# Kernel optimization log

Hardware: AMD Instinct MI355X
Metric: run time of the kernel (lower is better)

## Reference

```python
import jax, jax.numpy as jnp
import numpy as np

B, T, U = 4, 256, 64
D_ENC, D_DEC = 640, 640
INNER, VOCAB = 640, 1024


def setup_inputs() -> dict:
    key = jax.random.key(0)
    k1, k2, k3, k4, k5, k6 = jax.random.split(key, 6)
    return {
        "enc_state": jax.random.normal(k1, (B, T, D_ENC), jnp.float32),
        "dec_state": jax.random.normal(k2, (B, U, D_DEC), jnp.float32),
        # forward_layer: Linear(input_size=1280 -> inner=640); stored as [in, out]
        "w1": jax.random.normal(k3, (D_ENC + D_DEC, INNER), jnp.float32) * (1.0 / np.sqrt(D_ENC + D_DEC)),
        "b1": jax.random.normal(k4, (INNER,), jnp.float32) * 0.02,
        # project_layer: Linear(inner=640 -> vocab=1024)
        "w2": jax.random.normal(k5, (INNER, VOCAB), jnp.float32) * (1.0 / np.sqrt(INNER)),
        "b2": jax.random.normal(k6, (VOCAB,), jnp.float32) * 0.02,
    }


def reference(enc_state, dec_state, w1, b1, w2, b2):
    # Linear on concat([enc, dec]) == enc @ w1[:D_enc] + dec @ w1[D_enc:]
    # (same math as the torch repeat+cat+Linear, without materializing the
    #  [B,T,U,2D] concatenated grid)
    d_enc = enc_state.shape[-1]
    enc_proj = jnp.einsum('btd,dh->bth', enc_state, w1[:d_enc])   # [B,T,H]
    dec_proj = jnp.einsum('bud,dh->buh', dec_state, w1[d_enc:])   # [B,U,H]
    h = jnp.tanh(enc_proj[:, :, None, :] + dec_proj[:, None, :, :] + b1)  # [B,T,U,H]
    return jnp.einsum('btuh,hv->btuv', h, w2) + b2                # [B,T,U,V]
```

## Files before the change

kernel.cpp:

```cpp
#include <hip/hip_runtime.h>
#include <hip/hip_bf16.h>


typedef __attribute__((ext_vector_type(4))) float  f32x4;
typedef __attribute__((ext_vector_type(8))) __bf16 bf16x8;
typedef __attribute__((ext_vector_type(8))) unsigned short us8;

#define INNER 640
#define VOCAB 1024
#define M_TOT 65536
#define RE 1024
#define RD 256

#define ENCP_B (RE * INNER * 4)
#define DECP_B (RD * INNER * 4)
#define W2BT_B (VOCAB * INNER * 2)
#define HB_B   ((size_t)M_TOT * INNER * 2)
#define OFF_DECP ((size_t)ENCP_B)
#define OFF_W2BT (OFF_DECP + DECP_B)
#define OFF_HB   (OFF_W2BT + W2BT_B)
#define NEED_FULL (OFF_HB + HB_B)

__device__ __forceinline__ unsigned short f2bf(float f) {
    unsigned int u = __float_as_uint(f);
    u = (u + 0x7FFFu + ((u >> 16) & 1u)) >> 16;
    return (unsigned short)u;
}

__device__ __forceinline__ float fast_tanh(float x) {
    float e = __builtin_amdgcn_exp2f(x * 2.8853900817779268f);
    return 1.0f - 2.0f * __builtin_amdgcn_rcpf(e + 1.0f);
}

__device__ __forceinline__ void gl_lds16(const void* g, void* l) {
    __builtin_amdgcn_global_load_lds(
        (__attribute__((address_space(1))) void*)g,
        (__attribute__((address_space(3))) void*)l, 16, 0, 0);
}

__global__ __launch_bounds__(256) void prep_kernel(
        const float* __restrict__ enc, const float* __restrict__ dec,
        const float* __restrict__ w1, const float* __restrict__ b1,
        const float* __restrict__ w2,
        float* __restrict__ encp, float* __restrict__ decp,
        unsigned short* __restrict__ w2bT) {
    __shared__ __align__(16) char smem[64 * 65 * 4];
    int bx = blockIdx.x;
    int t = threadIdx.x;
    if (bx < 200) {
        float (*At)[68] = (float(*)[68])smem;
        float (*Bt)[68] = (float(*)[68])(smem + 16 * 68 * 4);
        const float* Ap; float* Op; const float* Wp; int mt, nt; bool isdec;
        if (bx < 160) { isdec = false; mt = bx / 10; nt = bx % 10; Ap = enc; Op = encp; Wp = w1; }
        else { isdec = true; int i = bx - 160; mt = i / 10; nt = i % 10; Ap = dec; Op = decp; Wp = w1 + 640 * 640; }
        int m0 = mt * 64, n0 = nt * 64;
        int tx = t & 15, ty = t >> 4;
        int ar = t >> 2, ac = t & 3;
        int br = t >> 4, bc = t & 15;
        float acc[4][4] = {};
        for (int k0 = 0; k0 < 640; k0 += 16) {
            f32x4 av = *(const f32x4*)&Ap[(m0 + ar) * 640 + k0 + ac * 4];
            f32x4 bv = *(const f32x4*)&Wp[(k0 + br) * 640 + n0 + bc * 4];
            __syncthreads();
            At[ac * 4 + 0][ar] = av[0]; At[ac * 4 + 1][ar] = av[1];
            At[ac * 4 + 2][ar] = av[2]; At[ac * 4 + 3][ar] = av[3];
            *(f32x4*)&Bt[br][bc * 4] = bv;
            __syncthreads();
            #pragma unroll
            for (int kk = 0; kk < 16; ++kk) {
                f32x4 a = *(const f32x4*)&At[kk][ty * 4];
                f32x4 b = *(const f32x4*)&Bt[kk][tx * 4];
                #pragma unroll
                for (int i = 0; i < 4; ++i)
                    #pragma unroll
                    for (int j = 0; j < 4; ++j)
                        acc[i][j] += a[i] * b[j];
            }
        }
        f32x4 bias = {0.f, 0.f, 0.f, 0.f};
        if (isdec) bias = *(const f32x4*)&b1[n0 + tx * 4];
        #pragma unroll
        for (int i = 0; i < 4; ++i) {
            f32x4 o;
            #pragma unroll
            for (int j = 0; j < 4; ++j) o[j] = acc[i][j] + bias[j];
            *(f32x4*)&Op[(m0 + ty * 4 + i) * 640 + n0 + nt * 0 + tx * 4] = o;
        }
    } else {
        float (*tile)[65] = (float(*)[65])smem;
        int i = bx - 200;
        int kt = i % 10, ntc = i / 10;
        int k0 = kt * 64, n0 = ntc * 64;
        #pragma unroll
        for (int p = 0; p < 4; ++p) {
            int id = t + p * 256;
            int r = id >> 4, c4 = id & 15;
            f32x4 v = *(const f32x4*)&w2[(k0 + r) * 1024 + n0 + c4 * 4];
            tile[r][c4 * 4 + 0] = v[0]; tile[r][c4 * 4 + 1] = v[1];
            tile[r][c4 * 4 + 2] = v[2]; tile[r][c4 * 4 + 3] = v[3];
        }
        __syncthreads();
        #pragma unroll
        for (int p = 0; p < 2; ++p) {
            int id = t + p * 256;
            int n = id >> 3, ch = id & 7;
            us8 hv;
            #pragma unroll
            for (int q = 0; q < 8; ++q) hv[q] = f2bf(tile[ch * 8 + q][n]);
            *(us8*)&w2bT[(n0 + n) * 640 + k0 + ch * 8] = hv;
        }
    }
}

__global__ __launch_bounds__(256) void hmat_kernel(
        const float* __restrict__ encp, const float* __restrict__ decp,
        unsigned short* __restrict__ Hb) {
    int c = blockIdx.x * 256 + threadIdx.x;
    int m = c / 80;
    int kc = (c - m * 80) * 8;
    int r1 = m >> 6;
    int r2 = ((m >> 14) << 6) | (m & 63);
    const float* ep = encp + r1 * 640 + kc;
    const float* dp = decp + r2 * 640 + kc;
    f32x4 e0 = *(const f32x4*)ep, e1 = *(const f32x4*)(ep + 4);
    f32x4 d0 = *(const f32x4*)dp, d1 = *(const f32x4*)(dp + 4);
    us8 hv;
    #pragma unroll
    for (int q = 0; q < 4; ++q) hv[q] = f2bf(fast_tanh(e0[q] + d0[q]));
    #pragma unroll
    for (int q = 0; q < 4; ++q) hv[4 + q] = f2bf(fast_tanh(e1[q] + d1[q]));
    *(us8*)&Hb[(size_t)m * 640 + kc] = hv;
}

template<int FUSED>
__global__ __launch_bounds__(256) void jgemm_kernel(
        const unsigned short* __restrict__ Hb, const unsigned short* __restrict__ w2bT,
        const float* __restrict__ encp, const float* __restrict__ decp,
        const float* __restrict__ b2, float* __restrict__ out) {
    __shared__ __align__(16) unsigned short As[128 * 32];
    __shared__ __align__(16) unsigned short Bs[128 * 32];
    int bx = blockIdx.x;
    int lb = ((bx & 7) << 9) | (bx >> 3);
    int nt = lb & 7, mt = lb >> 3;
    int m0 = mt << 7, n0 = nt << 7;
    int tid = threadIdx.x;
    int lane = tid & 63, wave = tid >> 6;
    int wr = (wave >> 1) * 64, wc = (wave & 1) * 64;
    f32x4 acc[4][4] = {};
    int fr = lane & 15, fk = (lane >> 4) << 3;

    for (int kt = 0; kt < 20; ++kt) {
        int k0 = kt << 5;
        __syncthreads();
        if constexpr (!FUSED) {
            #pragma unroll
            for (int j = 0; j < 2; ++j) {
                int srow = wave * 32 + j * 16 + (lane >> 2);
                const char* ag = (const char*)Hb + (size_t)(m0 + srow) * 1280 + k0 * 2 + (lane & 3) * 16;
                const char* bg = (const char*)w2bT + (size_t)(n0 + srow) * 1280 + k0 * 2 + (lane & 3) * 16;
                gl_lds16(ag, (void*)&As[(wave * 32 + j * 16) * 32]);
                gl_lds16(bg, (void*)&Bs[(wave * 32 + j * 16) * 32]);
            }
        } else {
            int row = tid >> 1, kh = tid & 1;
            int m = m0 + row;
            int r1g = m >> 6;
            int r2g = ((m >> 14) << 6) | (m & 63);
            const float* ep = encp + r1g * 640 + k0 + kh * 16;
            const float* dp = decp + r2g * 640 + k0 + kh * 16;
            f32x4 e0 = *(const f32x4*)ep,       e1 = *(const f32x4*)(ep + 4);
            f32x4 e2 = *(const f32x4*)(ep + 8), e3 = *(const f32x4*)(ep + 12);
            f32x4 q0 = *(const f32x4*)dp,       q1 = *(const f32x4*)(dp + 4);
            f32x4 q2 = *(const f32x4*)(dp + 8), q3 = *(const f32x4*)(dp + 12);
            us8 h0, h1;
            #pragma unroll
            for (int q = 0; q < 4; ++q) {
                h0[q]     = f2bf(fast_tanh(e0[q] + q0[q]));
                h0[4 + q] = f2bf(fast_tanh(e1[q] + q1[q]));
                h1[q]     = f2bf(fast_tanh(e2[q] + q2[q]));
                h1[4 + q] = f2bf(fast_tanh(e3[q] + q3[q]));
            }
            *(us8*)&As[row * 32 + kh * 16] = h0;
            *(us8*)&As[row * 32 + kh * 16 + 8] = h1;
            #pragma unroll
            for (int j = 0; j < 2; ++j) {
                int srow = wave * 32 + j * 16 + (lane >> 2);
                const char* bg = (const char*)w2bT + (size_t)(n0 + srow) * 1280 + k0 * 2 + (lane & 3) * 16;
                gl_lds16(bg, (void*)&Bs[(wave * 32 + j * 16) * 32]);
            }
        }
        __syncthreads();
        bf16x8 af[4], bf[4];
        #pragma unroll
        for (int i = 0; i < 4; ++i) {
            af[i] = *(const bf16x8*)&As[(wr + i * 16 + fr) * 32 + fk];
            bf[i] = *(const bf16x8*)&Bs[(wc + i * 16 + fr) * 32 + fk];
        }
        #pragma unroll
        for (int i = 0; i < 4; ++i)
            #pragma unroll
            for (int j = 0; j < 4; ++j)
                acc[i][j] = __builtin_amdgcn_mfma_f32_16x16x32_bf16(af[i], bf[j], acc[i][j], 0, 0, 0);
    }

    int ccol = lane & 15, crow = (lane >> 4) << 2;
    #pragma unroll
    for (int j = 0; j < 4; ++j) {
        int col = n0 + wc + j * 16 + ccol;
        float bb = b2[col];
        #pragma unroll
        for (int i = 0; i < 4; ++i) {
            int row = m0 + wr + i * 16 + crow;
            #pragma unroll
            for (int r = 0; r < 4; ++r)
                out[(size_t)(row + r) * 1024 + col] = acc[i][j][r] + bb;
        }
    }
}

extern "C" void kernel_launch(void* const* d_in, const int* in_sizes, int n_in,
                              void* d_out, int out_size, void* d_ws, size_t ws_size,
                              hipStream_t stream) {
    const float* enc = (const float*)d_in[0];
    const float* dec = (const float*)d_in[1];
    const float* w1  = (const float*)d_in[2];
    const float* b1  = (const float*)d_in[3];
    const float* w2  = (const float*)d_in[4];
    const float* b2  = (const float*)d_in[5];
    float* out = (float*)d_out;

    char* w = (char*)d_ws;
    float* encp = (float*)w;
    float* decp = (float*)(w + OFF_DECP);
    unsigned short* w2bT = (unsigned short*)(w + OFF_W2BT);
    unsigned short* Hb = (unsigned short*)(w + OFF_HB);

    prep_kernel<<<360, 256, 0, stream>>>(enc, dec, w1, b1, w2, encp, decp, w2bT);
    if (ws_size >= NEED_FULL) {
        hmat_kernel<<<20480, 256, 0, stream>>>(encp, decp, Hb);
        jgemm_kernel<0><<<4096, 256, 0, stream>>>(Hb, w2bT, encp, decp, b2, out);
    } else {
        jgemm_kernel<1><<<4096, 256, 0, stream>>>(Hb, w2bT, encp, decp, b2, out);
    }
}
```

Baseline: 462.7 us.

## Replace bf16 GEMM with 256x256-tile, 4-stage pipelined async-load kernel

The unfused path's projection GEMM moves from 128x128 tiles with 256 threads to 256x256 tiles with 512 threads, 8 waves each owning a 128x64 sub-tile. A 4-deep LDS ring is filled with global-to-LDS loads issued three tiles ahead. Explicit vmcnt waits, barriers and setprio around the MFMA block let the loads overlap with compute. This raises operand reuse per LDS byte and hides global latency. The cost is about 128KB of LDS per block, which limits occupancy, and more accumulator registers. The fused fallback is split into its own kernel without functional change.

```diff
diff --git a/kernel.cpp b/kernel.cpp
--- a/kernel.cpp
+++ b/kernel.cpp
@@ -84,7 +84,7 @@
             f32x4 o;
             #pragma unroll
             for (int j = 0; j < 4; ++j) o[j] = acc[i][j] + bias[j];
-            *(f32x4*)&Op[(m0 + ty * 4 + i) * 640 + n0 + nt * 0 + tx * 4] = o;
+            *(f32x4*)&Op[(m0 + ty * 4 + i) * 640 + n0 + tx * 4] = o;
         }
     } else {
         float (*tile)[65] = (float(*)[65])smem;
@@ -132,9 +132,84 @@
     *(us8*)&Hb[(size_t)m * 640 + kc] = hv;
 }
 
-template<int FUSED>
-__global__ __launch_bounds__(256) void jgemm_kernel(
+__global__ __launch_bounds__(512, 2) void jgemm256_kernel(
         const unsigned short* __restrict__ Hb, const unsigned short* __restrict__ w2bT,
+        const float* __restrict__ b2, float* __restrict__ out) {
+    __shared__ __align__(16) unsigned short sA[4][256 * 32];
+    __shared__ __align__(16) unsigned short sB[4][256 * 32];
+    int bx = blockIdx.x;
+    int lb = ((bx & 7) << 7) | (bx >> 3);
+    int nt = lb & 3, mt = lb >> 2;
+    int m0 = mt << 8, n0 = nt << 8;
+    int tid = threadIdx.x;
+    int lane = tid & 63, wave = tid >> 6;
+    int wm = wave >> 2, wn = wave & 3;
+
+    const char* HbBase = (const char*)Hb + (size_t)(m0 + (tid >> 2)) * 1280 + (tid & 3) * 16;
+    const char* WbBase = (const char*)w2bT + (size_t)(n0 + (tid >> 2)) * 1280 + (tid & 3) * 16;
+
+    f32x4 acc[8][4] = {};
+    int fr = lane & 15, fk8 = (lane >> 4) << 3;
+    int arow0 = (wm << 7) + fr;
+    int brow0 = (wn << 6) + fr;
+
+#define STAGE_TILE(tt) do { \
+    unsigned short* As_ = sA[(tt) & 3]; unsigned short* Bs_ = sB[(tt) & 3]; \
+    const char* ga_ = HbBase + (tt) * 64; \
+    const char* gb_ = WbBase + (tt) * 64; \
+    gl_lds16(ga_,          (void*)(As_ + wave * 512)); \
+    gl_lds16(ga_ + 163840, (void*)(As_ + 4096 + wave * 512)); \
+    gl_lds16(gb_,          (void*)(Bs_ + wave * 512)); \
+    gl_lds16(gb_ + 163840, (void*)(Bs_ + 4096 + wave * 512)); \
+} while (0)
+
+#define JTILE(t_, VN_, DOST_) do { \
+    asm volatile("s_waitcnt vmcnt(%0)" :: "i"(VN_) : "memory"); \
+    __builtin_amdgcn_s_barrier(); \
+    __builtin_amdgcn_sched_barrier(0); \
+    if (DOST_) STAGE_TILE((t_) + 3); \
+    const unsigned short* As_r = sA[(t_) & 3]; \
+    const unsigned short* Bs_r = sB[(t_) & 3]; \
+    bf16x8 af[8], bfv[4]; \
+    _Pragma("unroll") for (int ri = 0; ri < 8; ++ri) \
+        af[ri] = *(const bf16x8*)&As_r[(arow0 + ri * 16) * 32 + fk8]; \
+    _Pragma("unroll") for (int ci = 0; ci < 4; ++ci) \
+        bfv[ci] = *(const bf16x8*)&Bs_r[(brow0 + ci * 16) * 32 + fk8]; \
+    __builtin_amdgcn_s_setprio(1); \
+    _Pragma("unroll") for (int ri = 0; ri < 8; ++ri) \
+        _Pragma("unroll") for (int ci = 0; ci < 4; ++ci) \
+            acc[ri][ci] = __builtin_amdgcn_mfma_f32_16x16x32_bf16(af[ri], bfv[ci], acc[ri][ci], 0, 0, 0); \
+    __builtin_amdgcn_s_setprio(0); \
+} while (0)
+
+    STAGE_TILE(0); STAGE_TILE(1); STAGE_TILE(2);
+    for (int t = 0; t < 17; ++t) {
+        JTILE(t, 8, true);
+    }
+    JTILE(17, 8, false);
+    JTILE(18, 4, false);
+    JTILE(19, 0, false);
+
+#undef JTILE
+#undef STAGE_TILE
+
+    int crow = (lane >> 4) << 2;
+    #pragma unroll
+    for (int ci = 0; ci < 4; ++ci) {
+        int col = n0 + (wn << 6) + ci * 16 + fr;
+        float bb = b2[col];
+        #pragma unroll
+        for (int ri = 0; ri < 8; ++ri) {
+            int row = m0 + (wm << 7) + ri * 16 + crow;
+            #pragma unroll
+            for (int r = 0; r < 4; ++r)
+                out[(size_t)(row + r) * 1024 + col] = acc[ri][ci][r] + bb;
+        }
+    }
+}
+
+__global__ __launch_bounds__(256) void jgemm_fused_kernel(
+        const unsigned short* __restrict__ w2bT,
         const float* __restrict__ encp, const float* __restrict__ decp,
         const float* __restrict__ b2, float* __restrict__ out) {
     __shared__ __align__(16) unsigned short As[128 * 32];
@@ -148,46 +223,34 @@
     int wr = (wave >> 1) * 64, wc = (wave & 1) * 64;
     f32x4 acc[4][4] = {};
     int fr = lane & 15, fk = (lane >> 4) << 3;
-
     for (int kt = 0; kt < 20; ++kt) {
         int k0 = kt << 5;
         __syncthreads();
-        if constexpr (!FUSED) {
-            #pragma unroll
-            for (int j = 0; j < 2; ++j) {
-                int srow = wave * 32 + j * 16 + (lane >> 2);
-                const char* ag = (const char*)Hb + (size_t)(m0 + srow) * 1280 + k0 * 2 + (lane & 3) * 16;
-                const char* bg = (const char*)w2bT + (size_t)(n0 + srow) * 1280 + k0 * 2 + (lane & 3) * 16;
-                gl_lds16(ag, (void*)&As[(wave * 32 + j * 16) * 32]);
-                gl_lds16(bg, (void*)&Bs[(wave * 32 + j * 16) * 32]);
-            }
-        } else {
-            int row = tid >> 1, kh = tid & 1;
-            int m = m0 + row;
-            int r1g = m >> 6;
-            int r2g = ((m >> 14) << 6) | (m & 63);
-            const float* ep = encp + r1g * 640 + k0 + kh * 16;
-            const float* dp = decp + r2g * 640 + k0 + kh * 16;
-            f32x4 e0 = *(const f32x4*)ep,       e1 = *(const f32x4*)(ep + 4);
-            f32x4 e2 = *(const f32x4*)(ep + 8), e3 = *(const f32x4*)(ep + 12);
-            f32x4 q0 = *(const f32x4*)dp,       q1 = *(const f32x4*)(dp + 4);
-            f32x4 q2 = *(const f32x4*)(dp + 8), q3 = *(const f32x4*)(dp + 12);
-            us8 h0, h1;
-            #pragma unroll
-            for (int q = 0; q < 4; ++q) {
-                h0[q]     = f2bf(fast_tanh(e0[q] + q0[q]));
-                h0[4 + q] = f2bf(fast_tanh(e1[q] + q1[q]));
-                h1[q]     = f2bf(fast_tanh(e2[q] + q2[q]));
-                h1[4 + q] = f2bf(fast_tanh(e3[q] + q3[q]));
-            }
-            *(us8*)&As[row * 32 + kh * 16] = h0;
-            *(us8*)&As[row * 32 + kh * 16 + 8] = h1;
-            #pragma unroll
-            for (int j = 0; j < 2; ++j) {
-                int srow = wave * 32 + j * 16 + (lane >> 2);
-                const char* bg = (const char*)w2bT + (size_t)(n0 + srow) * 1280 + k0 * 2 + (lane & 3) * 16;
-                gl_lds16(bg, (void*)&Bs[(wave * 32 + j * 16) * 32]);
-            }
+        int row = tid >> 1, kh = tid & 1;
+        int m = m0 + row;
+        int r1g = m >> 6;
+        int r2g = ((m >> 14) << 6) | (m & 63);
+        const float* ep = encp + r1g * 640 + k0 + kh * 16;
+        const float* dp = decp + r2g * 640 + k0 + kh * 16;
+        f32x4 e0 = *(const f32x4*)ep,       e1 = *(const f32x4*)(ep + 4);
+        f32x4 e2 = *(const f32x4*)(ep + 8), e3 = *(const f32x4*)(ep + 12);
+        f32x4 q0 = *(const f32x4*)dp,       q1 = *(const f32x4*)(dp + 4);
+        f32x4 q2 = *(const f32x4*)(dp + 8), q3 = *(const f32x4*)(dp + 12);
+        us8 h0, h1;
+        #pragma unroll
+        for (int q = 0; q < 4; ++q) {
+            h0[q]     = f2bf(fast_tanh(e0[q] + q0[q]));
+            h0[4 + q] = f2bf(fast_tanh(e1[q] + q1[q]));
+            h1[q]     = f2bf(fast_tanh(e2[q] + q2[q]));
+            h1[4 + q] = f2bf(fast_tanh(e3[q] + q3[q]));
+        }
+        *(us8*)&As[row * 32 + kh * 16] = h0;
+        *(us8*)&As[row * 32 + kh * 16 + 8] = h1;
+        #pragma unroll
+        for (int j = 0; j < 2; ++j) {
+            int srow = wave * 32 + j * 16 + (lane >> 2);
+            const char* bg = (const char*)w2bT + (size_t)(n0 + srow) * 1280 + k0 * 2 + (lane & 3) * 16;
+            gl_lds16(bg, (void*)&Bs[(wave * 32 + j * 16) * 32]);
         }
         __syncthreads();
         bf16x8 af[4], bf[4];
@@ -202,7 +265,6 @@
             for (int j = 0; j < 4; ++j)
                 acc[i][j] = __builtin_amdgcn_mfma_f32_16x16x32_bf16(af[i], bf[j], acc[i][j], 0, 0, 0);
     }
-
     int ccol = lane & 15, crow = (lane >> 4) << 2;
     #pragma unroll
     for (int j = 0; j < 4; ++j) {
@@ -238,8 +300,8 @@
     prep_kernel<<<360, 256, 0, stream>>>(enc, dec, w1, b1, w2, encp, decp, w2bT);
     if (ws_size >= NEED_FULL) {
         hmat_kernel<<<20480, 256, 0, stream>>>(encp, decp, Hb);
-        jgemm_kernel<0><<<4096, 256, 0, stream>>>(Hb, w2bT, encp, decp, b2, out);
+        jgemm256_kernel<<<1024, 512, 0, stream>>>(Hb, w2bT, b2, out);
     } else {
-        jgemm_kernel<1><<<4096, 256, 0, stream>>>(Hb, w2bT, encp, decp, b2, out);
-    }
-}
+        jgemm_fused_kernel<<<4096, 256, 0, stream>>>(w2bT, encp, decp, b2, out);
+    }
+}
```

New measurement: 457.6 us. No clear change (-1.1%).
